# Kernel optimization log

Hardware: AMD Instinct MI355X
Metric: run time of the kernel (lower is better)

The kernel has to match this reference:

```python
import jax, jax.numpy as jnp
import numpy as np

UNITS = 300
MDN_MIXES = 8  # Config.mdn_mixes: 3*8=24 MDN params + 1 length = 25-dim feedback
FEAT = 25
GATE_IN = 2 * FEAT  # concat(inputs, prev_output)


def setup_inputs() -> dict:
    key = jax.random.key(0)
    ks = jax.random.split(key, 12)
    B, T = 2048, 512
    x = jax.random.uniform(ks[0], (B, T, FEAT), dtype=jnp.float32)
    s = 0.05
    kernel = jax.random.normal(ks[1], (FEAT, 4 * UNITS), dtype=jnp.float32) * s
    recurrent_kernel = jax.random.normal(ks[2], (UNITS, 4 * UNITS), dtype=jnp.float32) * s
    # unit_forget_bias: zeros except forget-gate slice = ones
    bias = jnp.concatenate([
        jnp.zeros((UNITS,), jnp.float32),
        jnp.ones((UNITS,), jnp.float32),
        jnp.zeros((2 * UNITS,), jnp.float32),
    ])
    # MLPGate: 2-layer MLP combining the two 25-dim distributions -> 24-dim
    mlp_w1 = jax.random.normal(ks[3], (GATE_IN, GATE_IN), dtype=jnp.float32) * s
    mlp_b1 = jnp.zeros((GATE_IN,), jnp.float32)
    mlp_w2 = jax.random.normal(ks[4], (GATE_IN, FEAT - 1), dtype=jnp.float32) * s
    mlp_b2 = jnp.zeros((FEAT - 1,), jnp.float32)
    # MDN heads on h (units -> mdn_mixes each)
    wa = jax.random.normal(ks[5], (UNITS, MDN_MIXES), dtype=jnp.float32) * s
    ba = jnp.zeros((MDN_MIXES,), jnp.float32)
    wm = jax.random.normal(ks[6], (UNITS, MDN_MIXES), dtype=jnp.float32) * s
    bm = jnp.zeros((MDN_MIXES,), jnp.float32)
    ws = jax.random.normal(ks[7], (UNITS, MDN_MIXES), dtype=jnp.float32) * s
    bs = jnp.zeros((MDN_MIXES,), jnp.float32)
    return {
        'x': x, 'kernel': kernel, 'recurrent_kernel': recurrent_kernel, 'bias': bias,
        'mlp_w1': mlp_w1, 'mlp_b1': mlp_b1, 'mlp_w2': mlp_w2, 'mlp_b2': mlp_b2,
        'wa': wa, 'ba': ba, 'wm': wm, 'bm': bm, 'ws': ws, 'bs': bs,
    }


def _hard_sigmoid(z):
    return jnp.clip(0.2 * z + 0.5, 0.0, 1.0)


def _nnelu(z):
    return 1.0 + jax.nn.elu(z)


def reference(x, kernel, recurrent_kernel, bias,
              mlp_w1, mlp_b1, mlp_w2, mlp_b2,
              wa, ba, wm, bm, ws, bs):
    B = x.shape[0]
    dt = x.dtype

    def step(carry, xt):
        h, c, prev = carry  # [B,U], [B,U], [B,25]
        il = xt[:, 24:25]
        pl = prev[:, 24:25]
        combined = il + pl
        denom = jnp.maximum(combined, jnp.asarray(1e-8, dt))  # LengthNormalizer
        inp2 = jnp.concatenate([xt[:, :24], il / denom], axis=1)
        prev2 = jnp.concatenate([prev[:, :24], pl / denom], axis=1)
        # MLP gate combining the two distributions
        g = jax.nn.relu(jnp.concatenate([inp2, prev2], axis=1) @ mlp_w1 + mlp_b1)
        g = g @ mlp_w2 + mlp_b2  # [B,24]
        gate_out = jnp.concatenate([g, combined], axis=1)  # [B,25]
        # LSTM gates (split-kernel math == fused without dropout)
        z = gate_out @ kernel + h @ recurrent_kernel + bias  # [B,4U]
        zi, zf, zc, zo = jnp.split(z, 4, axis=1)
        i = _hard_sigmoid(zi)
        f = _hard_sigmoid(zf)
        o = _hard_sigmoid(zo)
        c_new = f * c + i * jnp.tanh(zc)
        h_new = o * jnp.tanh(c_new)
        # MDN heads
        alpha = jax.nn.softmax(h_new @ wa + ba, axis=-1)
        mu = h_new @ wm + bm
        sigma = _nnelu(h_new @ ws + bs)
        mdn = jnp.concatenate([alpha, mu, sigma, combined], axis=1)  # [B,25]
        return (h_new, c_new, mdn), mdn

    h0 = jnp.zeros((B, UNITS), dt)
    c0 = jnp.zeros((B, UNITS), dt)
    prev0 = jnp.zeros((B, FEAT), dt)
    xt = jnp.swapaxes(x, 0, 1)  # [T,B,25]
    _, ys = jax.lax.scan(step, (h0, c0, prev0), xt)
    return jnp.swapaxes(ys, 0, 1)  # [B,T,25]
```

## Files before the change

kernel.cpp:

```cpp
#include <hip/hip_runtime.h>
#include <math.h>

#define BB 2048
#define TT 512
#define NFEAT 25
#define UNITS 300
#define RPB 16
#define NBLK (BB/RPB)
#define NT 512
#define NKS 11
#define TPW 10
#define AROW 360
#define F8ROW 352
#define GROW 72

#define OFF_B0 0
#define SZ_B0  (8*TPW*512)
#define OFF_M1 (OFF_B0 + SZ_B0)
#define SZ_M1  (4*2*512)
#define OFF_M2 (OFF_M1 + SZ_M1)
#define SZ_M2  (2*2*512)
#define OFF_H  (OFF_M2 + SZ_M2)
#define SZ_H   (2*NKS*512)
#define OFF_F8 (OFF_H + SZ_H)
#define SZ_F8B (8*100*512)
#define SW_SZ  (SZ_M1 + SZ_M2 + SZ_H)
#define SWM1   0
#define SWM2   (SZ_M1)
#define SWH    (SZ_M1 + SZ_M2)

typedef __attribute__((ext_vector_type(4))) float f32x4;
typedef __attribute__((ext_vector_type(8))) short bf16x8;
typedef long long ll8;

static __device__ __forceinline__ unsigned short f2bf(float f) {
    union { float f; unsigned u; } x; x.f = f;
    unsigned r = (x.u + 0x7fffu + ((x.u >> 16) & 1u)) >> 16;
    return (unsigned short)r;
}
static __device__ __forceinline__ unsigned char f2f8(float f) {
    return (unsigned char)(__builtin_amdgcn_cvt_pk_fp8_f32(f, 0.f, 0, false) & 0xff);
}
static __device__ __forceinline__ float ftanh(float v) {
    float e = __builtin_amdgcn_exp2f(v * 2.8853900817779268f);
    return 1.f - 2.f * __builtin_amdgcn_rcpf(e + 1.f);
}
static __device__ __forceinline__ int zcol(int c) { return (c & 3) * 300 + (c >> 2); }

__global__ __launch_bounds__(256) void conv_b0(
    const float* __restrict__ wk, unsigned short* __restrict__ dst)
{
    int idx = blockIdx.x * 256 + threadIdx.x;
    if (idx >= SZ_B0) return;
    int j = idx & 7, n = (idx >> 3) & 15, kg = (idx >> 7) & 3, q = idx >> 9;
    int i = q % TPW, w = q / TPW;
    int k = kg * 8 + j, c = (w + 8 * i) * 16 + n;
    float v = (k < 25 && c < 1200) ? wk[k * 1200 + zcol(c)] : 0.f;
    dst[OFF_B0 + idx] = f2bf(v);
}

__global__ __launch_bounds__(256) void conv_b8(
    const float* __restrict__ wr, unsigned char* __restrict__ dst8)
{
    int idx = blockIdx.x * 256 + threadIdx.x;
    if (idx >= SZ_F8B) return;
    int j = idx & 7, n = (idx >> 3) & 15, kg = (idx >> 7) & 3, q = idx >> 9;
    int i = q % TPW, ks1 = (q / TPW) % 10, w = q / 100;
    int k = (ks1 + 1) * 32 + kg * 8 + j, c = (w + 8 * i) * 16 + n;
    float v = (k >= 32 && k < 332 && c < 1200) ? wr[(k - 32) * 1200 + zcol(c)] : 0.f;
    dst8[idx] = f2f8(v);
}

__global__ __launch_bounds__(256) void conv_gen(
    const float* __restrict__ W, unsigned short* __restrict__ dst,
    int K, int N, int nks, int total)
{
    int idx = blockIdx.x * 256 + threadIdx.x;
    if (idx >= total) return;
    int j = idx & 7, n = (idx >> 3) & 15, kg = (idx >> 7) & 3, qq = idx >> 9;
    int ks = qq % nks, nt = qq / nks;
    int k = ks * 32 + kg * 8 + j, col = nt * 16 + n;
    float v = (k < K && col < N) ? W[k * N + col] : 0.f;
    dst[idx] = f2bf(v);
}

__global__ __launch_bounds__(256) void conv_heads(
    const float* __restrict__ wa, const float* __restrict__ wm,
    const float* __restrict__ wsg, unsigned short* __restrict__ dst)
{
    int idx = blockIdx.x * 256 + threadIdx.x;
    if (idx >= SZ_H) return;
    int j = idx & 7, n = (idx >> 3) & 15, kg = (idx >> 7) & 3, qq = idx >> 9;
    int ks = qq % NKS, nt = qq / NKS;
    int k = ks * 32 + kg * 8 + j, col = nt * 16 + n;
    float v = 0.f;
    if (k >= 32 && k < 332 && col < 24) {
        int u = k - 32, h = col >> 3, m = col & 7;
        const float* W = (h == 0) ? wa : (h == 1) ? wm : wsg;
        v = W[u * 8 + m];
    }
    dst[OFF_H + idx] = f2bf(v);
}

#define MFMA   __builtin_amdgcn_mfma_f32_16x16x32_bf16
#define MFMA8  __builtin_amdgcn_mfma_f32_16x16x32_fp8_fp8
#define LOG2E  1.4426950408889634f

__global__ __launch_bounds__(NT, 2)
void dilstm(
    const float* __restrict__ x,
    const unsigned short* __restrict__ wf,
    const float* __restrict__ bz,
    const float* __restrict__ b1v,
    const float* __restrict__ b2v,
    const float* __restrict__ ba,
    const float* __restrict__ bm,
    const float* __restrict__ bs,
    float* __restrict__ out)
{
    __shared__ unsigned short Abf[2][RPB][AROW];
    __shared__ __attribute__((aligned(16))) unsigned char Af8[2][RPB][F8ROW];
    __shared__ unsigned short Gbf[RPB][GROW];
    __shared__ unsigned short G1b[RPB][GROW];
    __shared__ float Sc[RPB][24];
    __shared__ float Sc2[RPB][24];
    __shared__ float BzS[1280];
    __shared__ float Zw[8][2][16][20];
    __shared__ unsigned short SW[SW_SZ];

    const int t = threadIdx.x;
    const int lane = t & 63, wv = t >> 6;
    const int arow = lane & 15, akg = lane >> 4;
    const int crow0 = akg * 4;
    const int u_l = lane & 3, rr = lane >> 2;
    const int row0 = blockIdx.x * RPB;

    for (int i = t; i < 2 * RPB * AROW; i += NT) ((unsigned short*)Abf)[i] = 0;
    for (int i = t; i < 2 * RPB * F8ROW; i += NT) ((unsigned char*)Af8)[i] = 0;
    for (int i = t; i < RPB * GROW; i += NT) { ((unsigned short*)Gbf)[i] = 0; ((unsigned short*)G1b)[i] = 0; }
    for (int i = t; i < SW_SZ; i += NT) SW[i] = wf[OFF_M1 + i];
    for (int i = t; i < 1280; i += NT)
        BzS[i] = (i < 1200) ? bz[zcol(i)] : 0.f;

    float m1bias = 0.f, m2bias = 0.f, hbias = 0.f;
    {
        int c1 = wv * 16 + arow;
        if (wv < 4 && c1 < 50) m1bias = b1v[c1];
        if (wv < 2 && c1 < 24) {
            m2bias = b2v[c1];
            hbias = (c1 < 8) ? ba[c1] : (c1 < 16) ? bm[c1 - 8] : bs[c1 - 16];
        }
    }

    float creg[TPW];
    #pragma unroll
    for (int i = 0; i < TPW; ++i) creg[i] = 0.f;

    const unsigned short* bw0 = wf + OFF_B0 + wv * (TPW * 512) + (lane << 3);
    const unsigned char*  bw8 = (const unsigned char*)(wf + OFF_F8) + (size_t)wv * (100 * 512) + (lane << 3);

    const int rA = t / 25, eA = t - (t / 25) * 25;
    float combreg = 0.f, xreg = 0.f;
    if (t < RPB * NFEAT) xreg = x[((size_t)(row0 + rA) * TT) * NFEAT + eA];
    __syncthreads();

    if (t < RPB * NFEAT) {
        if (eA < 24) {
            Gbf[rA][eA] = f2bf(xreg);
        } else {
            float comb = xreg;
            combreg = comb;
            float denom = fmaxf(comb, 1e-8f);
            Gbf[rA][24] = f2bf(xreg / denom);
            Abf[0][rA][24] = f2bf(comb);
        }
    }
    __syncthreads();

    for (int ts = 0; ts < TT; ++ts) {
        const int p = ts & 1;

        bf16x8 bb0[TPW];
        ll8 bbA[TPW];
        #pragma unroll
        for (int i = 0; i < TPW; ++i)
            bb0[i] = *(const bf16x8*)(bw0 + i * 512);
        #pragma unroll
        for (int i = 0; i < TPW; ++i)
            bbA[i] = *(const ll8*)(bw8 + i * 512);
        if (t < RPB * NFEAT && ts + 1 < TT)
            xreg = x[((size_t)(row0 + rA) * TT + (ts + 1)) * NFEAT + eA];

        if (wv < 4) {
            bf16x8 a0 = *(const bf16x8*)&Gbf[arow][akg * 8];
            bf16x8 a1 = *(const bf16x8*)&Gbf[arow][32 + akg * 8];
            bf16x8 b0 = *(const bf16x8*)&SW[SWM1 + (wv * 2 + 0) * 512 + (lane << 3)];
            bf16x8 b1 = *(const bf16x8*)&SW[SWM1 + (wv * 2 + 1) * 512 + (lane << 3)];
            f32x4 acc1 = {0.f, 0.f, 0.f, 0.f};
            acc1 = MFMA(a0, b0, acc1, 0, 0, 0);
            acc1 = MFMA(a1, b1, acc1, 0, 0, 0);
            int col = wv * 16 + arow;
            if (col < 50) {
                #pragma unroll
                for (int rg = 0; rg < 4; ++rg)
                    G1b[crow0 + rg][col] = f2bf(fmaxf(acc1[rg] + m1bias, 0.f));
            }
        }
        __syncthreads();

        if (wv < 2) {
            bf16x8 a0 = *(const bf16x8*)&G1b[arow][akg * 8];
            bf16x8 a1 = *(const bf16x8*)&G1b[arow][32 + akg * 8];
            bf16x8 b0 = *(const bf16x8*)&SW[SWM2 + (wv * 2 + 0) * 512 + (lane << 3)];
            bf16x8 b1 = *(const bf16x8*)&SW[SWM2 + (wv * 2 + 1) * 512 + (lane << 3)];
            f32x4 acc2 = {0.f, 0.f, 0.f, 0.f};
            acc2 = MFMA(a0, b0, acc2, 0, 0, 0);
            acc2 = MFMA(a1, b1, acc2, 0, 0, 0);
            int col = wv * 16 + arow;
            if (col < 24) {
                #pragma unroll
                for (int rg = 0; rg < 4; ++rg)
                    Abf[p][crow0 + rg][col] = f2bf(acc2[rg] + m2bias);
            }
        }
        __syncthreads();

        {
            f32x4 acc[TPW];
            #pragma unroll
            for (int i = 0; i < TPW; ++i) acc[i] = (f32x4){0.f, 0.f, 0.f, 0.f};

            {
                bf16x8 aA = *(const bf16x8*)&Abf[p][arow][akg * 8];
                #pragma unroll
                for (int i = 0; i < TPW; ++i)
                    acc[i] = MFMA(aA, bb0[i], acc[i], 0, 0, 0);
            }
            {
                const unsigned char* af8p = &Af8[p][0][0] + arow * F8ROW + akg * 8;
                const unsigned char* bp = bw8;
                ll8 bbB[TPW];
                #pragma unroll 1
                for (int pr = 0; pr < 5; ++pr) {
                    const int ks = 2 * pr + 1;
                    #pragma unroll
                    for (int i = 0; i < TPW; ++i)
                        bbB[i] = *(const ll8*)(bp + 5120 + i * 512);
                    ll8 a8a = *(const ll8*)(af8p + ks * 32);
                    #pragma unroll
                    for (int i = 0; i < TPW; ++i)
                        acc[i] = MFMA8(a8a, bbA[i], acc[i], 0, 0, 0);
                    if (pr < 4) {
                        #pragma unroll
                        for (int i = 0; i < TPW; ++i)
                            bbA[i] = *(const ll8*)(bp + 10240 + i * 512);
                    }
                    ll8 a8b = *(const ll8*)(af8p + ks * 32 + 32);
                    #pragma unroll
                    for (int i = 0; i < TPW; ++i)
                        acc[i] = MFMA8(a8b, bbB[i], acc[i], 0, 0, 0);
                    bp += 10240;
                }
            }

            *(f32x4*)&Zw[wv][0][arow][crow0] = acc[0];
            #pragma unroll
            for (int i = 0; i < TPW; ++i) {
                if (i + 1 < TPW)
                    *(f32x4*)&Zw[wv][(i + 1) & 1][arow][crow0] = acc[i + 1];
                f32x4 bz4 = *(const f32x4*)&BzS[(wv + 8 * i) * 16 + 4 * u_l];
                const float* zp = &Zw[wv][i & 1][4 * u_l][rr];
                float zi = zp[0]  + bz4[0];
                float zf = zp[20] + bz4[1];
                float zc = zp[40] + bz4[2];
                float zo = zp[60] + bz4[3];
                if (wv + 8 * i < 75) {
                    float ig = fminf(fmaxf(0.2f * zi + 0.5f, 0.f), 1.f);
                    float fg = fminf(fmaxf(0.2f * zf + 0.5f, 0.f), 1.f);
                    float og = fminf(fmaxf(0.2f * zo + 0.5f, 0.f), 1.f);
                    float cn = fg * creg[i] + ig * ftanh(zc);
                    creg[i] = cn;
                    float hn = og * ftanh(cn);
                    int hc = 32 + (wv + 8 * i) * 4 + u_l;
                    Abf[p ^ 1][rr][hc] = f2bf(hn);
                    Af8[p ^ 1][rr][hc] = f2f8(hn);
                }
            }
        }
        __syncthreads();

        if (wv < 4) {
            const int ct = wv & 1, half = wv >> 1;
            const int k0 = 1 + 5 * half;
            f32x4 acc3 = {0.f, 0.f, 0.f, 0.f};
            #pragma unroll
            for (int ks = k0; ks < k0 + 5; ++ks) {
                bf16x8 a = *(const bf16x8*)&Abf[p ^ 1][arow][ks * 32 + akg * 8];
                bf16x8 b = *(const bf16x8*)&SW[SWH + (ct * NKS + ks) * 512 + (lane << 3)];
                acc3 = MFMA(a, b, acc3, 0, 0, 0);
            }
            int col = ct * 16 + arow;
            if (col < 24) {
                if (half == 0) {
                    #pragma unroll
                    for (int rg = 0; rg < 4; ++rg)
                        Sc[crow0 + rg][col] = acc3[rg] + hbias;
                } else {
                    #pragma unroll
                    for (int rg = 0; rg < 4; ++rg)
                        Sc2[crow0 + rg][col] = acc3[rg];
                }
            }
        }
        __syncthreads();

        if (t < RPB * NFEAT) {
            float v;
            if (eA < 8) {
                float s0 = Sc[rA][0] + Sc2[rA][0];
                float mx = s0;
                float sv[8]; sv[0] = s0;
                #pragma unroll
                for (int m = 1; m < 8; ++m) {
                    sv[m] = Sc[rA][m] + Sc2[rA][m];
                    mx = fmaxf(mx, sv[m]);
                }
                float sum = 0.f;
                #pragma unroll
                for (int m = 0; m < 8; ++m)
                    sum += __builtin_amdgcn_exp2f((sv[m] - mx) * LOG2E);
                v = __builtin_amdgcn_exp2f((sv[eA] - mx) * LOG2E) / sum;
            } else if (eA < 16) {
                v = Sc[rA][eA] + Sc2[rA][eA];
            } else if (eA < 24) {
                float s = Sc[rA][eA] + Sc2[rA][eA];
                v = (s > 0.f) ? (1.f + s) : __builtin_amdgcn_exp2f(s * LOG2E);
            } else {
                v = combreg;
            }
            out[((size_t)(row0 + rA) * TT + ts) * NFEAT + eA] = v;
            if (eA < 24) {
                Gbf[rA][eA]      = f2bf(xreg);
                Gbf[rA][25 + eA] = f2bf(v);
            } else {
                float comb = xreg + combreg;
                float denom = fmaxf(comb, 1e-8f);
                Gbf[rA][24] = f2bf(xreg / denom);
                Gbf[rA][49] = f2bf(combreg / denom);
                Abf[p ^ 1][rA][24] = f2bf(comb);
                combreg = comb;
            }
        }
        __syncthreads();
    }
}

extern "C" void kernel_launch(void* const* d_in, const int* in_sizes, int n_in,
                              void* d_out, int out_size, void* d_ws, size_t ws_size,
                              hipStream_t stream) {
    const float* x   = (const float*)d_in[0];
    const float* wk  = (const float*)d_in[1];
    const float* wr  = (const float*)d_in[2];
    const float* bz  = (const float*)d_in[3];
    const float* w1  = (const float*)d_in[4];
    const float* b1  = (const float*)d_in[5];
    const float* w2  = (const float*)d_in[6];
    const float* b2  = (const float*)d_in[7];
    const float* wa  = (const float*)d_in[8];
    const float* ba  = (const float*)d_in[9];
    const float* wm  = (const float*)d_in[10];
    const float* bm  = (const float*)d_in[11];
    const float* wsg = (const float*)d_in[12];
    const float* bs  = (const float*)d_in[13];
    float* out = (float*)d_out;
    unsigned short* wf = (unsigned short*)d_ws;
    unsigned char*  wf8 = (unsigned char*)(wf + OFF_F8);

    conv_b0<<<(SZ_B0 + 255) / 256, 256, 0, stream>>>(wk, wf);
    conv_b8<<<(SZ_F8B + 255) / 256, 256, 0, stream>>>(wr, wf8);
    conv_gen<<<(SZ_M1 + 255) / 256, 256, 0, stream>>>(w1, wf + OFF_M1, 50, 50, 2, SZ_M1);
    conv_gen<<<(SZ_M2 + 255) / 256, 256, 0, stream>>>(w2, wf + OFF_M2, 50, 24, 2, SZ_M2);
    conv_heads<<<(SZ_H + 255) / 256, 256, 0, stream>>>(wa, wm, wsg, wf);
    dilstm<<<NBLK, NT, 0, stream>>>(x, wf, bz, b1, b2, ba, bm, bs, out);
}
```

Baseline: 3.923 ms.

## Move input-kernel MFMA to FP8 and apply combined-length term in FP32

The per-step input projection (24 MLP-gate features times the input kernel) now uses FP8 MFMA with FP8 weights and an FP8 activation buffer instead of bf16. This halves the weight bytes streamed from global memory each step. The length column is removed from that GEMM and added in FP32 as comb*wk during the gate epilogue, with weights staged in shared memory. The bf16 h buffer is no longer double-buffered. The head biases are folded into the head GEMM through a constant-one column. FP8 for the MLP output lowers precision.

```diff
diff --git a/kernel.cpp b/kernel.cpp
--- a/kernel.cpp
+++ b/kernel.cpp
@@ -10,19 +10,22 @@
 #define NT 512
 #define NKS 11
 #define TPW 10
-#define AROW 360
-#define F8ROW 352
+#define HROW 360
+#define F8ROW 392
+#define G2ROW 40
 #define GROW 72
 
-#define OFF_B0 0
-#define SZ_B0  (8*TPW*512)
-#define OFF_M1 (OFF_B0 + SZ_B0)
+#define OFF_M1 0
 #define SZ_M1  (4*2*512)
 #define OFF_M2 (OFF_M1 + SZ_M1)
 #define SZ_M2  (2*2*512)
 #define OFF_H  (OFF_M2 + SZ_M2)
 #define SZ_H   (2*NKS*512)
-#define OFF_F8 (OFF_H + SZ_H)
+#define OFF_BZ (OFF_H + SZ_H)
+#define OFF_WK (OFF_BZ + 2560)
+#define OFF_B08 (OFF_WK + 2560)
+#define SZ_B08B (8*TPW*512)
+#define OFF_F8 (OFF_B08 + 20480)
 #define SZ_F8B (8*100*512)
 #define SW_SZ  (SZ_M1 + SZ_M2 + SZ_H)
 #define SWM1   0
@@ -47,16 +50,16 @@
 }
 static __device__ __forceinline__ int zcol(int c) { return (c & 3) * 300 + (c >> 2); }
 
-__global__ __launch_bounds__(256) void conv_b0(
-    const float* __restrict__ wk, unsigned short* __restrict__ dst)
+__global__ __launch_bounds__(256) void conv_b08(
+    const float* __restrict__ wk, unsigned char* __restrict__ dst8)
 {
     int idx = blockIdx.x * 256 + threadIdx.x;
-    if (idx >= SZ_B0) return;
+    if (idx >= SZ_B08B) return;
     int j = idx & 7, n = (idx >> 3) & 15, kg = (idx >> 7) & 3, q = idx >> 9;
     int i = q % TPW, w = q / TPW;
     int k = kg * 8 + j, c = (w + 8 * i) * 16 + n;
-    float v = (k < 25 && c < 1200) ? wk[k * 1200 + zcol(c)] : 0.f;
-    dst[OFF_B0 + idx] = f2bf(v);
+    float v = (k < 24 && c < 1200) ? wk[k * 1200 + zcol(c)] : 0.f;
+    dst8[idx] = f2f8(v);
 }
 
 __global__ __launch_bounds__(256) void conv_b8(
@@ -71,6 +74,22 @@
     dst8[idx] = f2f8(v);
 }
 
+__global__ __launch_bounds__(256) void conv_misc(
+    const float* __restrict__ wk, const float* __restrict__ bz,
+    float* __restrict__ bzdst, float* __restrict__ wkdst)
+{
+    int i = blockIdx.x * 256 + threadIdx.x;
+    if (i >= 1280) return;
+    float vb = 0.f, vw = 0.f;
+    if (i < 1200) {
+        int oc = zcol(i);
+        vb = bz[oc];
+        vw = wk[24 * 1200 + oc];
+    }
+    bzdst[i] = vb;
+    wkdst[i] = vw;
+}
+
 __global__ __launch_bounds__(256) void conv_gen(
     const float* __restrict__ W, unsigned short* __restrict__ dst,
     int K, int N, int nks, int total)
@@ -86,7 +105,9 @@
 
 __global__ __launch_bounds__(256) void conv_heads(
     const float* __restrict__ wa, const float* __restrict__ wm,
-    const float* __restrict__ wsg, unsigned short* __restrict__ dst)
+    const float* __restrict__ wsg, const float* __restrict__ ba,
+    const float* __restrict__ bm, const float* __restrict__ bs,
+    unsigned short* __restrict__ dst)
 {
     int idx = blockIdx.x * 256 + threadIdx.x;
     if (idx >= SZ_H) return;
@@ -94,12 +115,16 @@
     int ks = qq % NKS, nt = qq / NKS;
     int k = ks * 32 + kg * 8 + j, col = nt * 16 + n;
     float v = 0.f;
-    if (k >= 32 && k < 332 && col < 24) {
-        int u = k - 32, h = col >> 3, m = col & 7;
-        const float* W = (h == 0) ? wa : (h == 1) ? wm : wsg;
-        v = W[u * 8 + m];
-    }
-    dst[OFF_H + idx] = f2bf(v);
+    if (col < 24) {
+        if (k >= 32 && k < 332) {
+            int u = k - 32, h = col >> 3, m = col & 7;
+            const float* W = (h == 0) ? wa : (h == 1) ? wm : wsg;
+            v = W[u * 8 + m];
+        } else if (k == 332) {
+            v = (col < 8) ? ba[col] : (col < 16) ? bm[col - 8] : bs[col - 16];
+        }
+    }
+    dst[idx] = f2bf(v);
 }
 
 #define MFMA   __builtin_amdgcn_mfma_f32_16x16x32_bf16
@@ -110,21 +135,20 @@
 void dilstm(
     const float* __restrict__ x,
     const unsigned short* __restrict__ wf,
-    const float* __restrict__ bz,
     const float* __restrict__ b1v,
     const float* __restrict__ b2v,
-    const float* __restrict__ ba,
-    const float* __restrict__ bm,
-    const float* __restrict__ bs,
     float* __restrict__ out)
 {
-    __shared__ unsigned short Abf[2][RPB][AROW];
+    __shared__ unsigned short Hbf[RPB][HROW];
     __shared__ __attribute__((aligned(16))) unsigned char Af8[2][RPB][F8ROW];
+    __shared__ __attribute__((aligned(16))) unsigned char G2b8[RPB][G2ROW];
     __shared__ unsigned short Gbf[RPB][GROW];
     __shared__ unsigned short G1b[RPB][GROW];
     __shared__ float Sc[RPB][24];
     __shared__ float Sc2[RPB][24];
     __shared__ float BzS[1280];
+    __shared__ float WkS[1280];
+    __shared__ float CombS[RPB];
     __shared__ float Zw[8][2][16][20];
     __shared__ unsigned short SW[SW_SZ];
 
@@ -135,29 +159,31 @@
     const int u_l = lane & 3, rr = lane >> 2;
     const int row0 = blockIdx.x * RPB;
 
-    for (int i = t; i < 2 * RPB * AROW; i += NT) ((unsigned short*)Abf)[i] = 0;
+    for (int i = t; i < RPB * HROW; i += NT) ((unsigned short*)Hbf)[i] = 0;
     for (int i = t; i < 2 * RPB * F8ROW; i += NT) ((unsigned char*)Af8)[i] = 0;
+    for (int i = t; i < RPB * G2ROW; i += NT) ((unsigned char*)G2b8)[i] = 0;
     for (int i = t; i < RPB * GROW; i += NT) { ((unsigned short*)Gbf)[i] = 0; ((unsigned short*)G1b)[i] = 0; }
     for (int i = t; i < SW_SZ; i += NT) SW[i] = wf[OFF_M1 + i];
-    for (int i = t; i < 1280; i += NT)
-        BzS[i] = (i < 1200) ? bz[zcol(i)] : 0.f;
-
-    float m1bias = 0.f, m2bias = 0.f, hbias = 0.f;
+    {
+        const float* bzp = (const float*)(wf + OFF_BZ);
+        const float* wkp = (const float*)(wf + OFF_WK);
+        for (int i = t; i < 1280; i += NT) { BzS[i] = bzp[i]; WkS[i] = wkp[i]; }
+    }
+    if (t < RPB) Hbf[t][332] = f2bf(1.f);
+
+    float m1bias = 0.f, m2bias = 0.f;
     {
         int c1 = wv * 16 + arow;
         if (wv < 4 && c1 < 50) m1bias = b1v[c1];
-        if (wv < 2 && c1 < 24) {
-            m2bias = b2v[c1];
-            hbias = (c1 < 8) ? ba[c1] : (c1 < 16) ? bm[c1 - 8] : bs[c1 - 16];
-        }
+        if (wv < 2 && c1 < 24) m2bias = b2v[c1];
     }
 
     float creg[TPW];
     #pragma unroll
     for (int i = 0; i < TPW; ++i) creg[i] = 0.f;
 
-    const unsigned short* bw0 = wf + OFF_B0 + wv * (TPW * 512) + (lane << 3);
-    const unsigned char*  bw8 = (const unsigned char*)(wf + OFF_F8) + (size_t)wv * (100 * 512) + (lane << 3);
+    const unsigned char* bw08 = (const unsigned char*)(wf + OFF_B08) + wv * (TPW * 512) + (lane << 3);
+    const unsigned char* bw8  = (const unsigned char*)(wf + OFF_F8) + (size_t)wv * (100 * 512) + (lane << 3);
 
     const int rA = t / 25, eA = t - (t / 25) * 25;
     float combreg = 0.f, xreg = 0.f;
@@ -172,7 +198,7 @@
             combreg = comb;
             float denom = fmaxf(comb, 1e-8f);
             Gbf[rA][24] = f2bf(xreg / denom);
-            Abf[0][rA][24] = f2bf(comb);
+            CombS[rA] = comb;
         }
     }
     __syncthreads();
@@ -180,11 +206,10 @@
     for (int ts = 0; ts < TT; ++ts) {
         const int p = ts & 1;
 
-        bf16x8 bb0[TPW];
-        ll8 bbA[TPW];
+        ll8 b08[TPW], bbA[TPW];
         #pragma unroll
         for (int i = 0; i < TPW; ++i)
-            bb0[i] = *(const bf16x8*)(bw0 + i * 512);
+            b08[i] = *(const ll8*)(bw08 + i * 512);
         #pragma unroll
         for (int i = 0; i < TPW; ++i)
             bbA[i] = *(const ll8*)(bw8 + i * 512);
@@ -220,7 +245,7 @@
             if (col < 24) {
                 #pragma unroll
                 for (int rg = 0; rg < 4; ++rg)
-                    Abf[p][crow0 + rg][col] = f2bf(acc2[rg] + m2bias);
+                    G2b8[crow0 + rg][col] = f2f8(acc2[rg] + m2bias);
             }
         }
         __syncthreads();
@@ -231,10 +256,10 @@
             for (int i = 0; i < TPW; ++i) acc[i] = (f32x4){0.f, 0.f, 0.f, 0.f};
 
             {
-                bf16x8 aA = *(const bf16x8*)&Abf[p][arow][akg * 8];
+                ll8 a8g = *(const ll8*)&G2b8[arow][akg * 8];
                 #pragma unroll
                 for (int i = 0; i < TPW; ++i)
-                    acc[i] = MFMA(aA, bb0[i], acc[i], 0, 0, 0);
+                    acc[i] = MFMA8(a8g, b08[i], acc[i], 0, 0, 0);
             }
             {
                 const unsigned char* af8p = &Af8[p][0][0] + arow * F8ROW + akg * 8;
@@ -263,17 +288,19 @@
                 }
             }
 
+            float cmb = CombS[rr];
             *(f32x4*)&Zw[wv][0][arow][crow0] = acc[0];
             #pragma unroll
             for (int i = 0; i < TPW; ++i) {
                 if (i + 1 < TPW)
                     *(f32x4*)&Zw[wv][(i + 1) & 1][arow][crow0] = acc[i + 1];
                 f32x4 bz4 = *(const f32x4*)&BzS[(wv + 8 * i) * 16 + 4 * u_l];
+                f32x4 wk4 = *(const f32x4*)&WkS[(wv + 8 * i) * 16 + 4 * u_l];
                 const float* zp = &Zw[wv][i & 1][4 * u_l][rr];
-                float zi = zp[0]  + bz4[0];
-                float zf = zp[20] + bz4[1];
-                float zc = zp[40] + bz4[2];
-                float zo = zp[60] + bz4[3];
+                float zi = zp[0]  + bz4[0] + cmb * wk4[0];
+                float zf = zp[20] + bz4[1] + cmb * wk4[1];
+                float zc = zp[40] + bz4[2] + cmb * wk4[2];
+                float zo = zp[60] + bz4[3] + cmb * wk4[3];
                 if (wv + 8 * i < 75) {
                     float ig = fminf(fmaxf(0.2f * zi + 0.5f, 0.f), 1.f);
                     float fg = fminf(fmaxf(0.2f * zf + 0.5f, 0.f), 1.f);
@@ -281,9 +308,9 @@
                     float cn = fg * creg[i] + ig * ftanh(zc);
                     creg[i] = cn;
                     float hn = og * ftanh(cn);
-                    int hc = 32 + (wv + 8 * i) * 4 + u_l;
-                    Abf[p ^ 1][rr][hc] = f2bf(hn);
-                    Af8[p ^ 1][rr][hc] = f2f8(hn);
+                    int hb = (wv + 8 * i) * 4 + u_l;
+                    Hbf[rr][32 + hb] = f2bf(hn);
+                    Af8[p ^ 1][rr][32 + hb] = f2f8(hn);
                 }
             }
         }
@@ -295,7 +322,7 @@
             f32x4 acc3 = {0.f, 0.f, 0.f, 0.f};
             #pragma unroll
             for (int ks = k0; ks < k0 + 5; ++ks) {
-                bf16x8 a = *(const bf16x8*)&Abf[p ^ 1][arow][ks * 32 + akg * 8];
+                bf16x8 a = *(const bf16x8*)&Hbf[arow][ks * 32 + akg * 8];
                 bf16x8 b = *(const bf16x8*)&SW[SWH + (ct * NKS + ks) * 512 + (lane << 3)];
                 acc3 = MFMA(a, b, acc3, 0, 0, 0);
             }
@@ -304,7 +331,7 @@
                 if (half == 0) {
                     #pragma unroll
                     for (int rg = 0; rg < 4; ++rg)
-                        Sc[crow0 + rg][col] = acc3[rg] + hbias;
+                        Sc[crow0 + rg][col] = acc3[rg];
                 } else {
                     #pragma unroll
                     for (int rg = 0; rg < 4; ++rg)
@@ -347,7 +374,7 @@
                 float denom = fmaxf(comb, 1e-8f);
                 Gbf[rA][24] = f2bf(xreg / denom);
                 Gbf[rA][49] = f2bf(combreg / denom);
-                Abf[p ^ 1][rA][24] = f2bf(comb);
+                CombS[rA] = comb;
                 combreg = comb;
             }
         }
@@ -374,12 +401,16 @@
     const float* bs  = (const float*)d_in[13];
     float* out = (float*)d_out;
     unsigned short* wf = (unsigned short*)d_ws;
-    unsigned char*  wf8 = (unsigned char*)(wf + OFF_F8);
-
-    conv_b0<<<(SZ_B0 + 255) / 256, 256, 0, stream>>>(wk, wf);
+    unsigned char*  wf08 = (unsigned char*)(wf + OFF_B08);
+    unsigned char*  wf8  = (unsigned char*)(wf + OFF_F8);
+    float* bzdst = (float*)(wf + OFF_BZ);
+    float* wkdst = (float*)(wf + OFF_WK);
+
+    conv_b08<<<(SZ_B08B + 255) / 256, 256, 0, stream>>>(wk, wf08);
     conv_b8<<<(SZ_F8B + 255) / 256, 256, 0, stream>>>(wr, wf8);
+    conv_misc<<<(1280 + 255) / 256, 256, 0, stream>>>(wk, bz, bzdst, wkdst);
     conv_gen<<<(SZ_M1 + 255) / 256, 256, 0, stream>>>(w1, wf + OFF_M1, 50, 50, 2, SZ_M1);
     conv_gen<<<(SZ_M2 + 255) / 256, 256, 0, stream>>>(w2, wf + OFF_M2, 50, 24, 2, SZ_M2);
-    conv_heads<<<(SZ_H + 255) / 256, 256, 0, stream>>>(wa, wm, wsg, wf);
-    dilstm<<<NBLK, NT, 0, stream>>>(x, wf, bz, b1, b2, ba, bm, bs, out);
-}
+    conv_heads<<<(SZ_H + 255) / 256, 256, 0, stream>>>(wa, wm, wsg, ba, bm, bs, wf + OFF_H);
+    dilstm<<<NBLK, NT, 0, stream>>>(x, wf, b1, b2, out);
+}
```

New measurement: 3.892 ms. Within noise of the previous version (-0.8%).
